# Performance work log

Measured on AMD Instinct MI355X. Metric: run time of the kernel, lower is better.

## Reference

```python
import jax, jax.numpy as jnp
import numpy as np

SIGMA = 45.0
N, M, D = 4096, 4096, 1024


def setup_inputs() -> dict:
    key = jax.random.key(0)
    k1, k2 = jax.random.split(key)
    inputs = jax.random.normal(k1, (N, D), dtype=jnp.float32)
    samples = jax.random.normal(k2, (M, D), dtype=jnp.float32)
    return {"inputs": inputs, "samples": samples}


def _sq_dists(x, y):
    # ||x_i||^2 + ||y_j||^2 - 2 x_i.y_j  -> [N, M]
    prod = x @ y.T
    xs = jnp.sum(x * x, axis=1)[:, None]
    ys = jnp.sum(y * y, axis=1)[None, :]
    return xs + ys - 2.0 * prod


def reference(inputs, samples):
    n = inputs.shape[0]
    m = samples.shape[0]
    x = inputs.reshape(n, -1)
    y = samples.reshape(m, -1)
    inv_s2 = 1.0 / (SIGMA ** 2)

    k_xx = _sq_dists(x, x)
    k_yy = _sq_dists(y, y)
    k_xy = _sq_dists(x, y)

    # unbiased MMD: exclude diagonal terms of k_xx, k_yy
    exx = jnp.exp(-k_xx * inv_s2)
    eyy = jnp.exp(-k_yy * inv_s2)
    exy = jnp.exp(-k_xy * inv_s2)

    mmd = (jnp.sum(exx) - jnp.sum(jnp.exp(-jnp.diag(k_xx) * inv_s2))) / (n * (n - 1))
    mmd = mmd + (jnp.sum(eyy) - jnp.sum(jnp.exp(-jnp.diag(k_yy) * inv_s2))) / (m * (m - 1))
    mmd = mmd - 2.0 / (n * m) * jnp.sum(exy)
    return mmd
```

## Files before the change

### kernel.cpp

```cpp
#include <hip/hip_runtime.h>
#include <math.h>


typedef _Float16 f16_t;
typedef _Float16 f16x4 __attribute__((ext_vector_type(4)));
typedef _Float16 f16x8 __attribute__((ext_vector_type(8)));
typedef float floatx4 __attribute__((ext_vector_type(4)));

#define NROWS 4096
#define MROWS 4096
#define DDIM  1024
#define BM    128
#define BK    32
#define TILE  (BM * BK)
#define NKT   (DDIM / BK)
#define PSTRIDE (4096 * BK)
#define NT    (NROWS / BM)
#define TRI   (NT * (NT + 1) / 2)
#define NBLK  (2 * TRI + NT * NT)

__global__ __launch_bounds__(256) void convert_kernel(
    const float* __restrict__ X, const float* __restrict__ Y,
    f16_t* __restrict__ Xp, f16_t* __restrict__ Yp,
    float* __restrict__ nx, float* __restrict__ ny) {
    const int wid  = threadIdx.x >> 6;
    const int lane = threadIdx.x & 63;
    const int row  = blockIdx.x * 4 + wid;
    const float* src;
    f16_t* dstp;
    float* nrm;
    int r;
    if (row < NROWS) {
        r = row;         src = X + (size_t)r * DDIM;
        dstp = Xp;  nrm = nx;
    } else {
        r = row - NROWS; src = Y + (size_t)r * DDIM;
        dstp = Yp;  nrm = ny;
    }
    const float4* s4 = (const float4*)src;
    float s = 0.f;
    #pragma unroll
    for (int c = 0; c < 4; c++) {
        float4 v = s4[c * 64 + lane];
        f16x4 h;
        h[0] = (f16_t)v.x; h[1] = (f16_t)v.y;
        h[2] = (f16_t)v.z; h[3] = (f16_t)v.w;
        *(f16x4*)(dstp + (size_t)(c * 8 + (lane >> 3)) * PSTRIDE
                       + (size_t)r * BK + (lane & 7) * 4) = h;
        float h0 = (float)h[0], h1 = (float)h[1];
        float h2 = (float)h[2], h3 = (float)h[3];
        s += h0 * h0 + h1 * h1 + h2 * h2 + h3 * h3;
    }
    #pragma unroll
    for (int off = 32; off > 0; off >>= 1) s += __shfl_down(s, off);
    if (lane == 0) nrm[r] = s;
}

__global__ __launch_bounds__(256) void mmd_mfma(
    const f16_t* __restrict__ Xp, const f16_t* __restrict__ Yp,
    const float* __restrict__ nx, const float* __restrict__ ny,
    double* __restrict__ partials) {
    __shared__ __align__(16) f16_t ldsA[TILE];
    __shared__ __align__(16) f16_t ldsB[TILE];
    __shared__ double wred[4];

    const int b = blockIdx.x;
    const f16_t *Ap, *Bp;
    const float *nA, *nB;
    int tr, tc;
    double coef;
    if (b < 2 * TRI) {
        int u = (b < TRI) ? b : b - TRI;
        int r = 0;
        while (u >= NT - r) { u -= NT - r; r++; }
        tr = r; tc = r + u;
        double w = (tr == tc) ? 1.0 : 2.0;
        if (b < TRI) { Ap = Xp; Bp = Xp; nA = nx; nB = nx;
                       coef = w / ((double)NROWS * (double)(NROWS - 1)); }
        else         { Ap = Yp; Bp = Yp; nA = ny; nB = ny;
                       coef = w / ((double)MROWS * (double)(MROWS - 1)); }
    } else {
        int u = b - 2 * TRI;
        tr = u >> 5; tc = u & 31;
        Ap = Xp; Bp = Yp; nA = nx; nB = ny;
        coef = -2.0 / ((double)NROWS * (double)MROWS);
    }

    const int t    = threadIdx.x;
    const int wave = t >> 6;
    const int lane = t & 63;
    const int wm   = wave >> 1;
    const int wn   = wave & 1;

    const int lr = lane >> 2;
    const int lc = (lane & 3) ^ ((lane >> 3) & 3);
    const f16_t* gsrc[4];
    f16_t* ldst[4];
    #pragma unroll
    for (int i = 0; i < 4; i++) {
        int idx = wave * 4 + i;
        int tile = idx >> 3;
        int rg   = idx & 7;
        const f16_t* base = tile ? (Bp + (size_t)tc * BM * BK)
                                 : (Ap + (size_t)tr * BM * BK);
        gsrc[i] = base + (size_t)(rg * 16 + lr) * BK + lc * 8;
        ldst[i] = (tile ? ldsB : ldsA) + rg * 16 * BK;
    }

    const int m    = lane & 15;
    const int quad = lane >> 4;
    const int sw8  = (quad ^ ((m >> 1) & 3)) * 8;

    float na[16], nb[4];
    #pragma unroll
    for (int i = 0; i < 4; i++) {
        #pragma unroll
        for (int r = 0; r < 4; r++)
            na[i * 4 + r] = nA[tr * BM + wm * 64 + i * 16 + quad * 4 + r];
        nb[i] = nB[tc * BM + wn * 64 + i * 16 + m];
    }

    floatx4 acc_r[4][4];
    #pragma unroll
    for (int i = 0; i < 4; i++)
        #pragma unroll
        for (int j = 0; j < 4; j++) acc_r[i][j] = (floatx4){0.f, 0.f, 0.f, 0.f};

    for (int kt = 0; kt < NKT; kt++) {
        const size_t ko = (size_t)kt * PSTRIDE;
        __syncthreads();
        #pragma unroll
        for (int i = 0; i < 4; i++) {
            __builtin_amdgcn_global_load_lds(
                (const __attribute__((address_space(1))) void*)(gsrc[i] + ko),
                (__attribute__((address_space(3))) void*)ldst[i],
                16, 0, 0);
        }
        __syncthreads();

        f16x8 ah[4], bh[4];
        #pragma unroll
        for (int s = 0; s < 4; s++) {
            ah[s] = *(const f16x8*)&ldsA[(wm * 64 + s * 16 + m) * BK + sw8];
            bh[s] = *(const f16x8*)&ldsB[(wn * 64 + s * 16 + m) * BK + sw8];
        }
        #pragma unroll
        for (int i = 0; i < 4; i++)
            #pragma unroll
            for (int j = 0; j < 4; j++)
                acc_r[i][j] = __builtin_amdgcn_mfma_f32_16x16x32_f16(ah[i], bh[j], acc_r[i][j], 0, 0, 0);
    }

    const float inv_s2 = 1.0f / 2025.0f;
    float lsum = 0.f;
    #pragma unroll
    for (int i = 0; i < 4; i++)
        #pragma unroll
        for (int j = 0; j < 4; j++)
            #pragma unroll
            for (int r = 0; r < 4; r++) {
                float arg = (2.f * acc_r[i][j][r] - na[i * 4 + r] - nb[j]) * inv_s2;
                lsum += __expf(arg);
            }

    double d = (double)lsum;
    #pragma unroll
    for (int off = 32; off > 0; off >>= 1) d += __shfl_down(d, off);
    if (lane == 0) wred[wave] = d;
    __syncthreads();
    if (t == 0)
        partials[b] = (wred[0] + wred[1] + wred[2] + wred[3]) * coef;
}

__global__ __launch_bounds__(256) void final_reduce(const double* __restrict__ partials,
                                                    float* __restrict__ out) {
    __shared__ double red[256];
    int t = threadIdx.x;
    double s = 0.0;
    for (int i = t; i < NBLK; i += 256) s += partials[i];
    red[t] = s;
    __syncthreads();
    for (int off = 128; off > 0; off >>= 1) {
        if (t < off) red[t] += red[t + off];
        __syncthreads();
    }
    if (t == 0) {
        double mmd = red[0] - 1.0 / (double)(NROWS - 1) - 1.0 / (double)(MROWS - 1);
        out[0] = (float)mmd;
    }
}

extern "C" void kernel_launch(void* const* d_in, const int* in_sizes, int n_in,
                              void* d_out, int out_size, void* d_ws, size_t ws_size,
                              hipStream_t stream) {
    const float* X = (const float*)d_in[0];
    const float* Y = (const float*)d_in[1];
    float* out = (float*)d_out;

    char* p = (char*)d_ws;
    double* partials = (double*)p;            p += ((size_t)NBLK * sizeof(double) + 255) & ~255ULL;
    float* nx = (float*)p;                    p += (size_t)NROWS * sizeof(float);
    float* ny = (float*)p;                    p += (size_t)MROWS * sizeof(float);
    f16_t* Xp = (f16_t*)p;                    p += (size_t)NROWS * DDIM * sizeof(f16_t);
    f16_t* Yp = (f16_t*)p;

    convert_kernel<<<(NROWS + MROWS) / 4, 256, 0, stream>>>(X, Y, Xp, Yp, nx, ny);
    mmd_mfma<<<NBLK, 256, 0, stream>>>(Xp, Yp, nx, ny, partials);
    final_reduce<<<1, 256, 0, stream>>>(partials, out);
}
```

Before: 155.6 us.

## Double K-tile depth to 64 with new swizzle and defer norm loads

Raises the K step per LDS tile from 32 to 64, so the convert kernel writes a 64-wide packed layout and the main loop runs half as many iterations. Each iteration now issues two rounds of MFMAs with a new XOR swizzle over eight 16-byte groups. This halves the number of barrier pairs and global-to-LDS load phases, at the cost of doubling LDS use per block. The row-norm loads also move from before the loop to the epilogue, using float4 reads, which frees registers while the loop runs.

New measurement: 164.7 us. 1.06x slower.

```diff
diff --git a/kernel.cpp b/kernel.cpp
--- a/kernel.cpp
+++ b/kernel.cpp
@@ -11,10 +11,10 @@
 #define MROWS 4096
 #define DDIM  1024
 #define BM    128
-#define BK    32
-#define TILE  (BM * BK)
-#define NKT   (DDIM / BK)
-#define PSTRIDE (4096 * BK)
+#define BKP   64
+#define TILE  (BM * BKP)
+#define NKT   (DDIM / BKP)
+#define PSTRIDE (4096 * BKP)
 #define NT    (NROWS / BM)
 #define TRI   (NT * (NT + 1) / 2)
 #define NBLK  (2 * TRI + NT * NT)
@@ -45,8 +45,8 @@
         f16x4 h;
         h[0] = (f16_t)v.x; h[1] = (f16_t)v.y;
         h[2] = (f16_t)v.z; h[3] = (f16_t)v.w;
-        *(f16x4*)(dstp + (size_t)(c * 8 + (lane >> 3)) * PSTRIDE
-                       + (size_t)r * BK + (lane & 7) * 4) = h;
+        *(f16x4*)(dstp + (size_t)(c * 4 + (lane >> 4)) * PSTRIDE
+                       + (size_t)r * BKP + (lane & 15) * 4) = h;
         float h0 = (float)h[0], h1 = (float)h[1];
         float h2 = (float)h[2], h3 = (float)h[3];
         s += h0 * h0 + h1 * h1 + h2 * h2 + h3 * h3;
@@ -92,45 +92,37 @@
     const int wm   = wave >> 1;
     const int wn   = wave & 1;
 
-    const int lr = lane >> 2;
-    const int lc = (lane & 3) ^ ((lane >> 3) & 3);
-    const f16_t* gsrc[4];
-    f16_t* ldst[4];
-    #pragma unroll
-    for (int i = 0; i < 4; i++) {
-        int idx = wave * 4 + i;
-        int tile = idx >> 3;
-        int rg   = idx & 7;
-        const f16_t* base = tile ? (Bp + (size_t)tc * BM * BK)
-                                 : (Ap + (size_t)tr * BM * BK);
-        gsrc[i] = base + (size_t)(rg * 16 + lr) * BK + lc * 8;
-        ldst[i] = (tile ? ldsB : ldsA) + rg * 16 * BK;
+    const int lr = lane >> 3;
+    const int lg = (lane & 7) ^ (lr & 7);
+    const f16_t* gsrc[8];
+    f16_t* ldst[8];
+    #pragma unroll
+    for (int i = 0; i < 8; i++) {
+        int idx = wave * 8 + i;
+        int tile = idx >> 4;
+        int rg   = idx & 15;
+        const f16_t* base = tile ? (Bp + (size_t)tc * BM * BKP)
+                                 : (Ap + (size_t)tr * BM * BKP);
+        gsrc[i] = base + (size_t)(rg * 8 + lr) * BKP + lg * 8;
+        ldst[i] = (tile ? ldsB : ldsA) + rg * 8 * BKP;
     }
 
     const int m    = lane & 15;
     const int quad = lane >> 4;
-    const int sw8  = (quad ^ ((m >> 1) & 3)) * 8;
-
-    float na[16], nb[4];
-    #pragma unroll
-    for (int i = 0; i < 4; i++) {
-        #pragma unroll
-        for (int r = 0; r < 4; r++)
-            na[i * 4 + r] = nA[tr * BM + wm * 64 + i * 16 + quad * 4 + r];
-        nb[i] = nB[tc * BM + wn * 64 + i * 16 + m];
-    }
-
-    floatx4 acc_r[4][4];
+    const int g0 = ((quad)     ^ (m & 7)) * 8;
+    const int g1 = ((4 + quad) ^ (m & 7)) * 8;
+
+    floatx4 acc[4][4];
     #pragma unroll
     for (int i = 0; i < 4; i++)
         #pragma unroll
-        for (int j = 0; j < 4; j++) acc_r[i][j] = (floatx4){0.f, 0.f, 0.f, 0.f};
+        for (int j = 0; j < 4; j++) acc[i][j] = (floatx4){0.f, 0.f, 0.f, 0.f};
 
     for (int kt = 0; kt < NKT; kt++) {
         const size_t ko = (size_t)kt * PSTRIDE;
         __syncthreads();
         #pragma unroll
-        for (int i = 0; i < 4; i++) {
+        for (int i = 0; i < 8; i++) {
             __builtin_amdgcn_global_load_lds(
                 (const __attribute__((address_space(1))) void*)(gsrc[i] + ko),
                 (__attribute__((address_space(3))) void*)ldst[i],
@@ -141,27 +133,42 @@
         f16x8 ah[4], bh[4];
         #pragma unroll
         for (int s = 0; s < 4; s++) {
-            ah[s] = *(const f16x8*)&ldsA[(wm * 64 + s * 16 + m) * BK + sw8];
-            bh[s] = *(const f16x8*)&ldsB[(wn * 64 + s * 16 + m) * BK + sw8];
+            ah[s] = *(const f16x8*)&ldsA[(wm * 64 + s * 16 + m) * BKP + g0];
+            bh[s] = *(const f16x8*)&ldsB[(wn * 64 + s * 16 + m) * BKP + g0];
         }
         #pragma unroll
         for (int i = 0; i < 4; i++)
             #pragma unroll
             for (int j = 0; j < 4; j++)
-                acc_r[i][j] = __builtin_amdgcn_mfma_f32_16x16x32_f16(ah[i], bh[j], acc_r[i][j], 0, 0, 0);
+                acc[i][j] = __builtin_amdgcn_mfma_f32_16x16x32_f16(ah[i], bh[j], acc[i][j], 0, 0, 0);
+        #pragma unroll
+        for (int s = 0; s < 4; s++) {
+            ah[s] = *(const f16x8*)&ldsA[(wm * 64 + s * 16 + m) * BKP + g1];
+            bh[s] = *(const f16x8*)&ldsB[(wn * 64 + s * 16 + m) * BKP + g1];
+        }
+        #pragma unroll
+        for (int i = 0; i < 4; i++)
+            #pragma unroll
+            for (int j = 0; j < 4; j++)
+                acc[i][j] = __builtin_amdgcn_mfma_f32_16x16x32_f16(ah[i], bh[j], acc[i][j], 0, 0, 0);
     }
 
     const float inv_s2 = 1.0f / 2025.0f;
+    float nbv[4];
+    #pragma unroll
+    for (int j = 0; j < 4; j++) nbv[j] = nB[tc * BM + wn * 64 + j * 16 + m];
     float lsum = 0.f;
     #pragma unroll
-    for (int i = 0; i < 4; i++)
+    for (int i = 0; i < 4; i++) {
+        float4 na4 = *(const float4*)&nA[tr * BM + wm * 64 + i * 16 + quad * 4];
         #pragma unroll
         for (int j = 0; j < 4; j++)
             #pragma unroll
             for (int r = 0; r < 4; r++) {
-                float arg = (2.f * acc_r[i][j][r] - na[i * 4 + r] - nb[j]) * inv_s2;
+                float arg = (2.f * acc[i][j][r] - (&na4.x)[r] - nbv[j]) * inv_s2;
                 lsum += __expf(arg);
             }
+    }
 
     double d = (double)lsum;
     #pragma unroll
```
